# Kernel tuning notes

Hardware: AMD Instinct MI355X
Metric: run time of the kernel (lower is better)

Reference implementation:

```python
import jax, jax.numpy as jnp
import numpy as np

EMB_DIM = 768
HEAD = 12
HEAD_DIM = EMB_DIM // HEAD


def setup_inputs() -> dict:
    key = jax.random.key(0)
    ks = jax.random.split(key, 6)
    B, N, D = 8, 1024, EMB_DIM
    s = 1.0 / np.sqrt(D)
    return {
        "z": jax.random.normal(ks[0], (B, N, D), dtype=jnp.float32),
        "w_q": jax.random.normal(ks[1], (D, D), dtype=jnp.float32) * s,
        "w_k": jax.random.normal(ks[2], (D, D), dtype=jnp.float32) * s,
        "w_v": jax.random.normal(ks[3], (D, D), dtype=jnp.float32) * s,
        "w_o": jax.random.normal(ks[4], (D, D), dtype=jnp.float32) * s,
        "b_o": jax.random.normal(ks[5], (D,), dtype=jnp.float32) * 0.01,
    }


def reference(z, w_q, w_k, w_v, w_o, b_o):
    B, N, D = z.shape
    sqrt_dh = jnp.asarray(HEAD_DIM, z.dtype) ** 0.5
    # project and split heads: [B, H, N, Dh]
    def heads(x, w):
        return (x @ w.T).reshape(B, N, HEAD, HEAD_DIM).transpose(0, 2, 1, 3)
    q = heads(z, w_q)
    k = heads(z, w_k)
    v = heads(z, w_v)
    dots = jnp.einsum("bhqd,bhkd->bhqk", q, k) / sqrt_dh
    attn = jax.nn.softmax(dots, axis=-1)  # dropout p=0 -> identity
    out = jnp.einsum("bhqk,bhkd->bhqd", attn, v)
    out = out.transpose(0, 2, 1, 3).reshape(B, N, D)
    return out @ w_o.T + b_o
```

## Files before the change

kernel.cpp:

```cpp
#include <hip/hip_runtime.h>
#include <hip/hip_bf16.h>
#include <stdint.h>

typedef unsigned short u16;
typedef __attribute__((ext_vector_type(8))) short bf16x8;
typedef __attribute__((ext_vector_type(4))) float f32x4;

__device__ __forceinline__ u16 f2bf(float f) {
    union { float f; unsigned int i; } c; c.f = f;
    unsigned int x = c.i;
    return (u16)((x + 0x7FFFu + ((x >> 16) & 1u)) >> 16);
}
__device__ __forceinline__ u16 f2bf_fast(float f) {
    union { float f; unsigned int i; } c; c.f = f;
    return (u16)((c.i + 0x8000u) >> 16);
}

__device__ __forceinline__ void glds16(const u16* g, u16* l) {
    __builtin_amdgcn_global_load_lds(
        (const __attribute__((address_space(1))) void*)g,
        (__attribute__((address_space(3))) void*)l, 16, 0, 0);
}

__global__ __launch_bounds__(256) void convert_all(
    const float* __restrict__ z, const float* __restrict__ wq,
    const float* __restrict__ wk, const float* __restrict__ wv,
    const float* __restrict__ wo,
    u16* __restrict__ zb, u16* __restrict__ wqb, u16* __restrict__ wkb,
    u16* __restrict__ wvb, u16* __restrict__ wob)
{
    int g = blockIdx.x * 256 + threadIdx.x;
    const float* s; u16* d;
    if (g < 786432)       { s = z;  d = zb;  }
    else if (g < 860160)  { s = wq; d = wqb; g -= 786432; }
    else if (g < 933888)  { s = wk; d = wkb; g -= 860160; }
    else if (g < 1007616) { s = wv; d = wvb; g -= 933888; }
    else                  { s = wo; d = wob; g -= 1007616; }
    float4 a = *(const float4*)(s + (size_t)g * 8);
    float4 b = *(const float4*)(s + (size_t)g * 8 + 4);
    u16 t[8] = {f2bf(a.x), f2bf(a.y), f2bf(a.z), f2bf(a.w),
                f2bf(b.x), f2bf(b.y), f2bf(b.z), f2bf(b.w)};
    *(uint4*)(d + (size_t)g * 8) = *(const uint4*)t;
}

template <int MI>
__device__ __forceinline__ void gemm_mainloop(
    const u16* __restrict__ A, const u16* __restrict__ B,
    u16* As, u16* Bs, f32x4 (&acc)[MI][4], int m0, int lda, int ldb, int K)
{
    const int t = threadIdx.x;
    const int w = t >> 6, lane = t & 63, quad = lane >> 4, lc = lane & 15;
    const int wm = w >> 1, wn = w & 1;
    const int swz = (lc >> 1) & 3;
    constexpr int NA = MI / 2;
    constexpr int ASZ = 1024 * MI;

    const u16* pa[NA]; int la[NA];
    #pragma unroll
    for (int j = 0; j < NA; j++) {
        const int c = j * 256 + t;
        const int row = c >> 2;
        const int kq = (c & 3) ^ ((row >> 1) & 3);
        pa[j] = &A[(size_t)(m0 + row) * lda + kq * 8];
        la[j] = (j * 256 + w * 64) * 8;
    }
    const u16* pb[2]; int lb[2];
    #pragma unroll
    for (int j = 0; j < 2; j++) {
        const int c = j * 256 + t;
        const int row = c >> 2;
        const int kq = (c & 3) ^ ((row >> 1) & 3);
        pb[j] = &B[(size_t)row * ldb + kq * 8];
        lb[j] = (j * 256 + w * 64) * 8;
    }

    #pragma unroll
    for (int j = 0; j < NA; j++) glds16(pa[j], As + la[j]);
    #pragma unroll
    for (int j = 0; j < 2; j++) glds16(pb[j], Bs + lb[j]);
    __syncthreads();

    int buf = 0;
    for (int k0 = 0; k0 < K; k0 += 32) {
        if (k0 + 32 < K) {
            const int na = (buf ^ 1) * ASZ, nbb = (buf ^ 1) * 4096;
            #pragma unroll
            for (int j = 0; j < NA; j++) glds16(pa[j] + k0 + 32, As + na + la[j]);
            #pragma unroll
            for (int j = 0; j < 2; j++)  glds16(pb[j] + k0 + 32, Bs + nbb + lb[j]);
        }
        bf16x8 af[MI], bfr[4];
        #pragma unroll
        for (int i = 0; i < MI; i++) {
            const int row = 32 * NA * wm + 16 * i + lc;
            af[i] = *(const bf16x8*)&As[buf * ASZ + (row * 4 + (quad ^ swz)) * 8];
        }
        #pragma unroll
        for (int j = 0; j < 4; j++) {
            const int row = 64 * wn + 16 * j + lc;
            bfr[j] = *(const bf16x8*)&Bs[buf * 4096 + (row * 4 + (quad ^ swz)) * 8];
        }
        #pragma unroll
        for (int i = 0; i < MI; i++)
            #pragma unroll
            for (int j = 0; j < 4; j++)
                acc[i][j] = __builtin_amdgcn_mfma_f32_16x16x32_bf16(af[i], bfr[j], acc[i][j], 0, 0, 0);
        __syncthreads();
        buf ^= 1;
    }
}

__global__ __launch_bounds__(256) void qkv_gemm(
    const u16* __restrict__ zb, const u16* __restrict__ wqb,
    const u16* __restrict__ wkb, const u16* __restrict__ wvb,
    u16* __restrict__ qkb, u16* __restrict__ vt)
{
    __shared__ __align__(16) u16 As[8192], Bs[8192];
    const int n0 = blockIdx.x * 128, m0 = blockIdx.y * 128;
    const u16* B;
    if (n0 < 768)       B = wqb + (size_t)n0 * 768;
    else if (n0 < 1536) B = wkb + (size_t)(n0 - 768) * 768;
    else                B = wvb + (size_t)(n0 - 1536) * 768;

    f32x4 acc[4][4] = {};
    gemm_mainloop<4>(zb, B, As, Bs, acc, m0, 768, 768, 768);

    const int t = threadIdx.x;
    const int w = t >> 6, lane = t & 63, quad = lane >> 4, lc = lane & 15;
    const int wm = w >> 1, wn = w & 1;

    if (n0 < 1536) {
        #pragma unroll
        for (int i = 0; i < 4; i++)
            #pragma unroll
            for (int j = 0; j < 4; j++) {
                const int col = n0 + 64 * wn + 16 * j + lc;
                #pragma unroll
                for (int r = 0; r < 4; r++) {
                    const int row = m0 + 64 * wm + 16 * i + quad * 4 + r;
                    qkb[(size_t)row * 1536 + col] = f2bf_fast(acc[i][j][r]);
                }
            }
    } else {
        #pragma unroll
        for (int i = 0; i < 4; i++)
            #pragma unroll
            for (int j = 0; j < 4; j++) {
                const int c = (n0 - 1536) + 64 * wn + 16 * j + lc;
                const int h = c >> 6, d = c & 63;
                const int tok0 = m0 + 64 * wm + 16 * i + quad * 4;
                const int b = tok0 >> 10, n = tok0 & 1023;
                ushort4 pk = { f2bf_fast(acc[i][j][0]), f2bf_fast(acc[i][j][1]),
                               f2bf_fast(acc[i][j][2]), f2bf_fast(acc[i][j][3]) };
                *(ushort4*)&vt[(((size_t)(b * 12 + h)) * 64 + d) * 1024 + n] = pk;
            }
    }
}

__global__ __launch_bounds__(256) void oproj_gemm(
    const u16* __restrict__ ob, const u16* __restrict__ wob,
    const float* __restrict__ bo, float* __restrict__ out)
{
    __shared__ __align__(16) u16 As[4096], Bs[8192];
    const int n0 = blockIdx.x * 128, m0 = blockIdx.y * 64;
    f32x4 acc[2][4] = {};
    gemm_mainloop<2>(ob, wob + (size_t)n0 * 768, As, Bs, acc, m0, 768, 768, 768);

    const int t = threadIdx.x;
    const int w = t >> 6, lane = t & 63, quad = lane >> 4, lc = lane & 15;
    const int wm = w >> 1, wn = w & 1;
    #pragma unroll
    for (int i = 0; i < 2; i++)
        #pragma unroll
        for (int j = 0; j < 4; j++) {
            const int col = n0 + 64 * wn + 16 * j + lc;
            const float bv = bo[col];
            #pragma unroll
            for (int r = 0; r < 4; r++) {
                const int row = m0 + 32 * wm + 16 * i + quad * 4 + r;
                out[(size_t)row * 768 + col] = acc[i][j][r] + bv;
            }
        }
}

__global__ __launch_bounds__(512, 4) void attn_kernel(
    const u16* __restrict__ qkb, const u16* __restrict__ vt,
    u16* __restrict__ obuf)
{
    const int b = blockIdx.x / 12, h = blockIdx.x % 12;
    const int q0 = blockIdx.y * 128;
    const int t = threadIdx.x;
    const int w = t >> 6, lane = t & 63, quad = lane >> 4, lc = lane & 15;

    const u16* Qp  = qkb + (size_t)b * 1024 * 1536 + h * 64;
    const u16* Kp  = Qp + 768;
    const u16* Vtp = vt + ((size_t)(b * 12 + h)) * 64 * 1024;

    __shared__ __align__(16) u16 U[128 * 136];
    __shared__ __align__(16) u16 Vts[64 * 128];

    const u16* kp[2]; u16* kl[2];
    #pragma unroll
    for (int j = 0; j < 2; j++) {
        const int c = j * 512 + t;
        const int row = c >> 3;
        const int kq = (c & 7) ^ ((row >> 1) & 7);
        kp[j] = Kp + (size_t)row * 1536 + kq * 8;
        kl[j] = &U[(j * 512 + w * 64) * 8];
    }

    bf16x8 qf[2];
    #pragma unroll
    for (int kk = 0; kk < 2; kk++)
        qf[kk] = *(const bf16x8*)&Qp[(size_t)(q0 + 16 * w + lc) * 1536 + kk * 32 + quad * 8];

    f32x4 oacc[4] = {};
    float lsum[4] = {0.0f, 0.0f, 0.0f, 0.0f};

    const float cs = 0.18033688011112042f;
    const int swk = (lc >> 1) & 7;

    for (int kt = 0; kt < 8; kt++) {
        const int kb = kt * 128;
        __syncthreads();
        #pragma unroll
        for (int j = 0; j < 2; j++)
            glds16(kp[j] + (size_t)kb * 1536, kl[j]);
        #pragma unroll
        for (int s2 = 0; s2 < 2; s2++) {
            const int s = 2 * w + s2;
            const int c = s * 64 + lane;
            const int d = c >> 4, kq = (c & 15) ^ (d & 15);
            glds16(&Vtp[(size_t)d * 1024 + kb + kq * 8], &Vts[s * 512]);
        }
        __syncthreads();

        f32x4 sacc[8] = {};
        #pragma unroll
        for (int j = 0; j < 8; j++) {
            const int nrow = 16 * j + lc;
            bf16x8 kf0 = *(const bf16x8*)&U[(nrow * 8 + (quad ^ swk)) * 8];
            bf16x8 kf1 = *(const bf16x8*)&U[(nrow * 8 + ((4 + quad) ^ swk)) * 8];
            sacc[j] = __builtin_amdgcn_mfma_f32_16x16x32_bf16(qf[0], kf0, sacc[j], 0, 0, 0);
            sacc[j] = __builtin_amdgcn_mfma_f32_16x16x32_bf16(qf[1], kf1, sacc[j], 0, 0, 0);
        }
        __syncthreads();

        #pragma unroll
        for (int j = 0; j < 8; j++)
            #pragma unroll
            for (int r = 0; r < 4; r++) {
                float p = __builtin_amdgcn_exp2f(sacc[j][r] * cs);
                lsum[r] += p;
                U[(16 * w + quad * 4 + r) * 136 + 16 * j + lc] = f2bf_fast(p);
            }

        #pragma unroll
        for (int ks = 0; ks < 4; ks++) {
            bf16x8 pa = *(const bf16x8*)&U[(16 * w + lc) * 136 + ks * 32 + quad * 8];
            #pragma unroll
            for (int jd = 0; jd < 4; jd++) {
                bf16x8 vb = *(const bf16x8*)&Vts[(((16 * jd + lc) << 4) + ((ks * 4 + quad) ^ lc)) * 8];
                oacc[jd] = __builtin_amdgcn_mfma_f32_16x16x32_bf16(pa, vb, oacc[jd], 0, 0, 0);
            }
        }
    }

    #pragma unroll
    for (int off = 1; off < 16; off <<= 1)
        #pragma unroll
        for (int r = 0; r < 4; r++)
            lsum[r] += __shfl_xor(lsum[r], off, 64);

    float invl[4];
    #pragma unroll
    for (int r = 0; r < 4; r++) invl[r] = __builtin_amdgcn_rcpf(lsum[r]);
    #pragma unroll
    for (int jd = 0; jd < 4; jd++)
        #pragma unroll
        for (int r = 0; r < 4; r++) {
            const int row = q0 + 16 * w + quad * 4 + r;
            const int col = h * 64 + 16 * jd + lc;
            obuf[((size_t)b * 1024 + row) * 768 + col] = f2bf_fast(oacc[jd][r] * invl[r]);
        }
}

extern "C" void kernel_launch(void* const* d_in, const int* in_sizes, int n_in,
                              void* d_out, int out_size, void* d_ws, size_t ws_size,
                              hipStream_t stream) {
    const float* z  = (const float*)d_in[0];
    const float* wq = (const float*)d_in[1];
    const float* wk = (const float*)d_in[2];
    const float* wv = (const float*)d_in[3];
    const float* wo = (const float*)d_in[4];
    const float* bo = (const float*)d_in[5];

    u16* ws16 = (u16*)d_ws;
    u16* zb   = ws16;
    u16* wqb  = zb  + 6291456;
    u16* wkb  = wqb + 589824;
    u16* wvb  = wkb + 589824;
    u16* wob  = wvb + 589824;
    u16* vt   = wob + 589824;
    u16* qkb  = (u16*)d_out;
    u16* obuf = zb;
    float* out = (float*)d_out;

    convert_all<<<4224, 256, 0, stream>>>(z, wq, wk, wv, wo, zb, wqb, wkb, wvb, wob);
    qkv_gemm<<<dim3(18, 64), 256, 0, stream>>>(zb, wqb, wkb, wvb, qkb, vt);
    attn_kernel<<<dim3(96, 8), 512, 0, stream>>>(qkb, vt, obuf);
    oproj_gemm<<<dim3(6, 128), 256, 0, stream>>>(obuf, wob, bo, out);
}
```

Before: 201.2 us.

## Triple-buffer GEMM mainloop with vmcnt waits and a single barrier per step

The shared GEMM mainloop moves from double to triple buffering of the A/B tiles in LDS. It prefetches two k-steps ahead and replaces the trailing __syncthreads with explicit s_waitcnt vmcnt counts plus one s_barrier per iteration. The aim is to hide global-to-LDS load latency behind the MFMAs and cut one barrier per iteration. LDS use per block grows by 50% in the QKV and O-projection kernels, which may lower occupancy. The hand-written vmcnt counts must match the number of outstanding loads per thread.

```diff
diff --git a/kernel.cpp b/kernel.cpp
--- a/kernel.cpp
+++ b/kernel.cpp
@@ -20,6 +20,13 @@
     __builtin_amdgcn_global_load_lds(
         (const __attribute__((address_space(1))) void*)g,
         (__attribute__((address_space(3))) void*)l, 16, 0, 0);
+}
+
+__device__ __forceinline__ void bar() { asm volatile("s_barrier" ::: "memory"); }
+template <int N> __device__ __forceinline__ void waitv() {
+    if constexpr (N == 0)      asm volatile("s_waitcnt vmcnt(0)" ::: "memory");
+    else if constexpr (N == 3) asm volatile("s_waitcnt vmcnt(3)" ::: "memory");
+    else if constexpr (N == 4) asm volatile("s_waitcnt vmcnt(4)" ::: "memory");
 }
 
 __global__ __launch_bounds__(256) void convert_all(
@@ -52,8 +59,10 @@
     const int w = t >> 6, lane = t & 63, quad = lane >> 4, lc = lane & 15;
     const int wm = w >> 1, wn = w & 1;
     const int swz = (lc >> 1) & 3;
-    constexpr int NA = MI / 2;
+    constexpr int NA  = MI / 2;
+    constexpr int GPT = NA + 2;
     constexpr int ASZ = 1024 * MI;
+    constexpr int BSZ = 4096;
 
     const u16* pa[NA]; int la[NA];
     #pragma unroll
@@ -77,36 +86,41 @@
     #pragma unroll
     for (int j = 0; j < NA; j++) glds16(pa[j], As + la[j]);
     #pragma unroll
-    for (int j = 0; j < 2; j++) glds16(pb[j], Bs + lb[j]);
-    __syncthreads();
-
-    int buf = 0;
-    for (int k0 = 0; k0 < K; k0 += 32) {
-        if (k0 + 32 < K) {
-            const int na = (buf ^ 1) * ASZ, nbb = (buf ^ 1) * 4096;
-            #pragma unroll
-            for (int j = 0; j < NA; j++) glds16(pa[j] + k0 + 32, As + na + la[j]);
-            #pragma unroll
-            for (int j = 0; j < 2; j++)  glds16(pb[j] + k0 + 32, Bs + nbb + lb[j]);
-        }
+    for (int j = 0; j < 2; j++)  glds16(pb[j], Bs + lb[j]);
+    #pragma unroll
+    for (int j = 0; j < NA; j++) glds16(pa[j] + 32, As + ASZ + la[j]);
+    #pragma unroll
+    for (int j = 0; j < 2; j++)  glds16(pb[j] + 32, Bs + BSZ + lb[j]);
+
+    const int nT = K >> 5;
+    for (int bk = 0; bk < nT; bk++) {
+        if (bk + 1 < nT) waitv<GPT>(); else waitv<0>();
+        bar();
+        if (bk + 2 < nT) {
+            const int wb = (bk + 2) % 3;
+            const int k2 = (bk + 2) * 32;
+            #pragma unroll
+            for (int j = 0; j < NA; j++) glds16(pa[j] + k2, As + wb * ASZ + la[j]);
+            #pragma unroll
+            for (int j = 0; j < 2; j++)  glds16(pb[j] + k2, Bs + wb * BSZ + lb[j]);
+        }
+        const int rb = bk % 3;
         bf16x8 af[MI], bfr[4];
         #pragma unroll
         for (int i = 0; i < MI; i++) {
             const int row = 32 * NA * wm + 16 * i + lc;
-            af[i] = *(const bf16x8*)&As[buf * ASZ + (row * 4 + (quad ^ swz)) * 8];
+            af[i] = *(const bf16x8*)&As[rb * ASZ + (row * 4 + (quad ^ swz)) * 8];
         }
         #pragma unroll
         for (int j = 0; j < 4; j++) {
             const int row = 64 * wn + 16 * j + lc;
-            bfr[j] = *(const bf16x8*)&Bs[buf * 4096 + (row * 4 + (quad ^ swz)) * 8];
+            bfr[j] = *(const bf16x8*)&Bs[rb * BSZ + (row * 4 + (quad ^ swz)) * 8];
         }
         #pragma unroll
         for (int i = 0; i < MI; i++)
             #pragma unroll
             for (int j = 0; j < 4; j++)
                 acc[i][j] = __builtin_amdgcn_mfma_f32_16x16x32_bf16(af[i], bfr[j], acc[i][j], 0, 0, 0);
-        __syncthreads();
-        buf ^= 1;
     }
 }
 
@@ -115,7 +129,7 @@
     const u16* __restrict__ wkb, const u16* __restrict__ wvb,
     u16* __restrict__ qkb, u16* __restrict__ vt)
 {
-    __shared__ __align__(16) u16 As[8192], Bs[8192];
+    __shared__ __align__(16) u16 As[12288], Bs[12288];
     const int n0 = blockIdx.x * 128, m0 = blockIdx.y * 128;
     const u16* B;
     if (n0 < 768)       B = wqb + (size_t)n0 * 768;
@@ -161,7 +175,7 @@
     const u16* __restrict__ ob, const u16* __restrict__ wob,
     const float* __restrict__ bo, float* __restrict__ out)
 {
-    __shared__ __align__(16) u16 As[4096], Bs[8192];
+    __shared__ __align__(16) u16 As[6144], Bs[12288];
     const int n0 = blockIdx.x * 128, m0 = blockIdx.y * 64;
     f32x4 acc[2][4] = {};
     gemm_mainloop<2>(ob, wob + (size_t)n0 * 768, As, Bs, acc, m0, 768, 768, 768);
```

After: 212.8 us. 5.8% more time.

## Widen QKV GEMM tile and pipeline async LDS loads with explicit vmcnt waits

Applied to the files above, without the earlier changes.

The QKV projection GEMM moves from 128x128 tiles with 256 threads to 128x256 tiles with 512 threads. It gets an inlined double-buffered main loop that issues global-to-LDS loads two K-steps ahead, and waits with raw s_waitcnt vmcnt plus s_barrier instead of __syncthreads. In the attention kernel, the V-tile load addresses are precomputed. The barrier waits only for the K loads (vmcnt(2)), so the V transfer can overlap the QK^T MFMAs. The aim is to hide global memory latency and raise reuse per block. The cost is more LDS and registers per block and fewer blocks in the QKV grid, and the hand-written waitcnt ordering must stay correct.

```diff
diff --git a/kernel.cpp b/kernel.cpp
--- a/kernel.cpp
+++ b/kernel.cpp
@@ -20,6 +20,13 @@
     __builtin_amdgcn_global_load_lds(
         (const __attribute__((address_space(1))) void*)g,
         (__attribute__((address_space(3))) void*)l, 16, 0, 0);
+}
+
+__device__ __forceinline__ void bar() { asm volatile("s_barrier" ::: "memory"); }
+template <int N> __device__ __forceinline__ void waitv() {
+    if constexpr (N == 0)      asm volatile("s_waitcnt vmcnt(0)" ::: "memory");
+    else if constexpr (N == 2) asm volatile("s_waitcnt vmcnt(2)" ::: "memory");
+    else if constexpr (N == 3) asm volatile("s_waitcnt vmcnt(3)" ::: "memory");
 }
 
 __global__ __launch_bounds__(256) void convert_all(
@@ -110,24 +117,73 @@
     }
 }
 
-__global__ __launch_bounds__(256) void qkv_gemm(
+__global__ __launch_bounds__(512) void qkv_gemm(
     const u16* __restrict__ zb, const u16* __restrict__ wqb,
     const u16* __restrict__ wkb, const u16* __restrict__ wvb,
     u16* __restrict__ qkb, u16* __restrict__ vt)
 {
-    __shared__ __align__(16) u16 As[8192], Bs[8192];
-    const int n0 = blockIdx.x * 128, m0 = blockIdx.y * 128;
-    const u16* B;
-    if (n0 < 768)       B = wqb + (size_t)n0 * 768;
-    else if (n0 < 1536) B = wkb + (size_t)(n0 - 768) * 768;
-    else                B = wvb + (size_t)(n0 - 1536) * 768;
-
-    f32x4 acc[4][4] = {};
-    gemm_mainloop<4>(zb, B, As, Bs, acc, m0, 768, 768, 768);
+    __shared__ __align__(16) u16 As[8192], Bs[16384];
+    const int n0 = blockIdx.x * 256, m0 = blockIdx.y * 128;
+    const u16* Bp;
+    if (n0 < 768)       Bp = wqb + (size_t)n0 * 768;
+    else if (n0 < 1536) Bp = wkb + (size_t)(n0 - 768) * 768;
+    else                Bp = wvb + (size_t)(n0 - 1536) * 768;
 
     const int t = threadIdx.x;
     const int w = t >> 6, lane = t & 63, quad = lane >> 4, lc = lane & 15;
-    const int wm = w >> 1, wn = w & 1;
+    const int wm = w >> 2, wn = w & 3;
+    const int swz = (lc >> 1) & 3;
+
+    const int rowA = t >> 2, kqA = (t & 3) ^ ((rowA >> 1) & 3);
+    const u16* pa = &zb[(size_t)(m0 + rowA) * 768 + kqA * 8];
+    const int laA = w * 512;
+    const u16* pb[2]; int lb[2];
+    #pragma unroll
+    for (int j = 0; j < 2; j++) {
+        const int c = j * 512 + t;
+        const int row = c >> 2;
+        const int kq = (c & 3) ^ ((row >> 1) & 3);
+        pb[j] = &Bp[(size_t)row * 768 + kq * 8];
+        lb[j] = (j * 512 + w * 64) * 8;
+    }
+
+    glds16(pa, As + laA);
+    glds16(pb[0], Bs + lb[0]);
+    glds16(pb[1], Bs + lb[1]);
+    glds16(pa + 32, As + 4096 + laA);
+    glds16(pb[0] + 32, Bs + 8192 + lb[0]);
+    glds16(pb[1] + 32, Bs + 8192 + lb[1]);
+
+    f32x4 acc[4][4] = {};
+    int buf = 0;
+    for (int bk = 0; bk < 24; bk++) {
+        if (bk + 1 < 24) waitv<3>(); else waitv<0>();
+        bar();
+        bf16x8 af[4], bfr[4];
+        #pragma unroll
+        for (int i = 0; i < 4; i++) {
+            const int row = 64 * wm + 16 * i + lc;
+            af[i] = *(const bf16x8*)&As[buf * 4096 + (row * 4 + (quad ^ swz)) * 8];
+        }
+        #pragma unroll
+        for (int j = 0; j < 4; j++) {
+            const int row = 64 * wn + 16 * j + lc;
+            bfr[j] = *(const bf16x8*)&Bs[buf * 8192 + (row * 4 + (quad ^ swz)) * 8];
+        }
+        #pragma unroll
+        for (int i = 0; i < 4; i++)
+            #pragma unroll
+            for (int j = 0; j < 4; j++)
+                acc[i][j] = __builtin_amdgcn_mfma_f32_16x16x32_bf16(af[i], bfr[j], acc[i][j], 0, 0, 0);
+        bar();
+        if (bk + 2 < 24) {
+            const int k2 = (bk + 2) * 32;
+            glds16(pa + k2, As + buf * 4096 + laA);
+            glds16(pb[0] + k2, Bs + buf * 8192 + lb[0]);
+            glds16(pb[1] + k2, Bs + buf * 8192 + lb[1]);
+        }
+        buf ^= 1;
+    }
 
     if (n0 < 1536) {
         #pragma unroll
@@ -208,6 +264,15 @@
         kp[j] = Kp + (size_t)row * 1536 + kq * 8;
         kl[j] = &U[(j * 512 + w * 64) * 8];
     }
+    const u16* vp[2]; u16* vl[2];
+    #pragma unroll
+    for (int s2 = 0; s2 < 2; s2++) {
+        const int s = 2 * w + s2;
+        const int c = s * 64 + lane;
+        const int d = c >> 4, kq = (c & 15) ^ (d & 15);
+        vp[s2] = Vtp + (size_t)d * 1024 + kq * 8;
+        vl[s2] = &Vts[s * 512];
+    }
 
     bf16x8 qf[2];
     #pragma unroll
@@ -220,20 +285,18 @@
     const float cs = 0.18033688011112042f;
     const int swk = (lc >> 1) & 7;
 
+    waitv<0>();
     for (int kt = 0; kt < 8; kt++) {
         const int kb = kt * 128;
-        __syncthreads();
+        bar();
         #pragma unroll
         for (int j = 0; j < 2; j++)
             glds16(kp[j] + (size_t)kb * 1536, kl[j]);
         #pragma unroll
-        for (int s2 = 0; s2 < 2; s2++) {
-            const int s = 2 * w + s2;
-            const int c = s * 64 + lane;
-            const int d = c >> 4, kq = (c & 15) ^ (d & 15);
-            glds16(&Vtp[(size_t)d * 1024 + kb + kq * 8], &Vts[s * 512]);
-        }
-        __syncthreads();
+        for (int s2 = 0; s2 < 2; s2++)
+            glds16(vp[s2] + kb, vl[s2]);
+        waitv<2>();
+        bar();
 
         f32x4 sacc[8] = {};
         #pragma unroll
@@ -244,7 +307,8 @@
             sacc[j] = __builtin_amdgcn_mfma_f32_16x16x32_bf16(qf[0], kf0, sacc[j], 0, 0, 0);
             sacc[j] = __builtin_amdgcn_mfma_f32_16x16x32_bf16(qf[1], kf1, sacc[j], 0, 0, 0);
         }
-        __syncthreads();
+        waitv<0>();
+        bar();
 
         #pragma unroll
         for (int j = 0; j < 8; j++)
@@ -307,7 +371,7 @@
     float* out = (float*)d_out;
 
     convert_all<<<4224, 256, 0, stream>>>(z, wq, wk, wv, wo, zb, wqb, wkb, wvb, wob);
-    qkv_gemm<<<dim3(18, 64), 256, 0, stream>>>(zb, wqb, wkb, wvb, qkb, vt);
+    qkv_gemm<<<dim3(9, 64), 512, 0, stream>>>(zb, wqb, wkb, wvb, qkb, vt);
     attn_kernel<<<dim3(96, 8), 512, 0, stream>>>(qkb, vt, obuf);
     oproj_gemm<<<dim3(6, 128), 256, 0, stream>>>(obuf, wob, bo, out);
 }
```

Result: no change. 200.2 us (-0.5%).
